# Performance work log

Measured on AMD Instinct MI355X. Metric: run time of the kernel, lower is better.

Reference implementation:

```python
import jax, jax.numpy as jnp
import numpy as np


def _cdist(x, y):
    # Euclidean pairwise distances, (N,D) x (M,D) -> (N,M)
    x2 = jnp.sum(x * x, axis=1, keepdims=True)          # (N,1)
    y2 = jnp.sum(y * y, axis=1, keepdims=True).T        # (1,M)
    sq = x2 + y2 - 2.0 * (x @ y.T)
    return jnp.sqrt(jnp.maximum(sq, 0.0))


def setup_inputs() -> dict:
    key = jax.random.key(0)
    k1, k2, k3, k4 = jax.random.split(key, 4)
    return {
        "pred_feat": jax.random.normal(k1, (8192, 6), dtype=jnp.float32),
        "pred_decoder": jax.random.normal(k2, (4096, 4), dtype=jnp.float32),
        "input_data": jax.random.normal(k3, (4096, 4), dtype=jnp.float32),
        "gt_data": jax.random.normal(k4, (32768, 6), dtype=jnp.float32),
    }


def _repulsion_loss(pred_points, alpha=100.0, margin=0.3):
    N = pred_points.shape[0]
    d = _cdist(pred_points, pred_points)                # (N,N)
    eye = jnp.eye(N, dtype=d.dtype)
    d_no_self = d + 1e6 * eye
    min_dist = jnp.min(d_no_self, axis=1)               # (N,)
    penalty = jax.nn.softplus(alpha * (margin - min_dist))
    return jnp.mean(penalty ** 2)


def reference(pred_feat, pred_decoder, input_data, gt_data):
    # train_decoder=False branch of CombinedCriterionAEImpulse.forward
    pred_points = pred_feat[:, :3]
    pred_normals = pred_feat[:, 3:]
    gt_points = gt_data[:, :3]
    gt_normals = gt_data[:, 3:]

    # nearest-neighbor matching: NxL cdist + argmin + gather
    dists = _cdist(pred_points, gt_points)              # (N,L)
    min_indices = jnp.argmin(dists, axis=1)             # (N,)
    closest_gt_points = gt_points[min_indices]          # (N,3)

    attraction_loss = jnp.mean((pred_points - closest_gt_points) ** 2)
    repulsion = _repulsion_loss(pred_points)
    inlier_loss = attraction_loss + repulsion

    # normal alignment loss
    closest_gt_normals = gt_normals[min_indices]        # (N,3)
    eps = 1e-05
    pn = pred_normals / jnp.maximum(
        jnp.linalg.norm(pred_normals, axis=1, keepdims=True), eps)
    gn = closest_gt_normals / jnp.maximum(
        jnp.linalg.norm(closest_gt_normals, axis=1, keepdims=True), eps)
    cos_theta = jnp.sum(pn * gn, axis=1)
    norm_loss = jnp.mean(1.0 - cos_theta)

    combined_loss = inlier_loss + norm_loss * 10.0
    return combined_loss
```

## Files before the change

kernel.cpp:

```cpp
#include <hip/hip_runtime.h>
#include <cstdint>

typedef unsigned short ushort_t;
typedef unsigned int u32;
typedef unsigned long long u64;
typedef __attribute__((ext_vector_type(8))) short bf16x8;
typedef __attribute__((ext_vector_type(16))) float f32x16;

#define N_PRED 8192
#define N_GT   32768

#define NN_WAVES  4096
#define ALL_WAVES 5120

#define O_PRA  1048576u
#define O_PRB  1310720u
#define O_KNN  1572864u
#define O_KRP  5767168u
#define O_PART 6815744u

__device__ __forceinline__ float max3f(float a, float b, float c) {
    float d;
    asm("v_max3_f32 %0, %1, %2, %3" : "=v"(d) : "v"(a), "v"(b), "v"(c));
    return d;
}
__device__ __forceinline__ ushort_t f2b(float v) {
    u32 b = __float_as_uint(v);
    return (ushort_t)((b + 0x7FFFu + ((b >> 16) & 1u)) >> 16);
}
__device__ __forceinline__ u32 packf(float v) {
    const u32 b = __float_as_uint(v);
    return b ^ ((u32)((int)b >> 31) | 0x80000000u);
}

#define LATCH(ACC, B, K, T)                                        \
    {                                                              \
        const float _m0 = max3f(ACC[0], ACC[1], ACC[2]);           \
        const float _m1 = max3f(ACC[3], ACC[4], ACC[5]);           \
        const float _m2 = max3f(ACC[6], ACC[7], ACC[8]);           \
        const float _m3 = max3f(ACC[9], ACC[10], ACC[11]);         \
        const float _m4 = max3f(ACC[12], ACC[13], ACC[14]);        \
        const float _m5 = max3f(_m0, _m1, ACC[15]);                \
        const float _m6 = max3f(_m2, _m3, _m4);                    \
        const float _gm = fmaxf(_m5, _m6);                         \
        K = (_gm > B) ? (u32)(T) : K;                              \
        B = fmaxf(B, _gm);                                         \
    }

#define MASKROW(ACC)                                               \
    {                                                              \
        _Pragma("unroll")                                          \
        for (int _r = 0; _r < 16; ++_r) {                          \
            const int _row = (_r & 3) + 8 * (_r >> 2) + rowoff;    \
            ACC[_r] = (_row == col) ? -3.0e38f : ACC[_r];          \
        }                                                          \
    }

__global__ __launch_bounds__(256) void k_prep(const float* __restrict__ pred,
                                              const float* __restrict__ gt,
                                              ushort_t* __restrict__ gtA,
                                              ushort_t* __restrict__ prA,
                                              ushort_t* __restrict__ prB) {
    const int i = blockIdx.x * 256 + threadIdx.x;
    if (i < N_GT) {
        const float x = gt[i * 6 + 0], y = gt[i * 6 + 1], z = gt[i * 6 + 2];
        const ushort_t xh = f2b(x), yh = f2b(y), zh = f2b(z);
        const ushort_t xl = f2b(x - __uint_as_float((u32)xh << 16));
        const ushort_t yl = f2b(y - __uint_as_float((u32)yh << 16));
        const ushort_t zl = f2b(z - __uint_as_float((u32)zh << 16));
        const float w = -0.5f * fmaf(z, z, fmaf(y, y, x * x));
        const ushort_t wh = f2b(w);
        const ushort_t wl = f2b(w - __uint_as_float((u32)wh << 16));
        ushort_t* d = gtA + (i >> 5) * 512 + (i & 31) * 8;
        d[0] = xh; d[1] = yh; d[2] = zh; d[3] = xh; d[4] = yh; d[5] = zh; d[6] = xl; d[7] = yl;
        d += 256;
        d[0] = zl; d[1] = wh; d[2] = wl; d[3] = 0; d[4] = 0; d[5] = 0; d[6] = 0; d[7] = 0;
    }
    if (i < N_PRED) {
        const float x = pred[i * 6 + 0], y = pred[i * 6 + 1], z = pred[i * 6 + 2];
        const ushort_t xh = f2b(x), yh = f2b(y), zh = f2b(z);
        const ushort_t xl = f2b(x - __uint_as_float((u32)xh << 16));
        const ushort_t yl = f2b(y - __uint_as_float((u32)yh << 16));
        const ushort_t zl = f2b(z - __uint_as_float((u32)zh << 16));
        const float w = -0.5f * fmaf(z, z, fmaf(y, y, x * x));
        const ushort_t wh = f2b(w);
        const ushort_t wl = f2b(w - __uint_as_float((u32)wh << 16));
        ushort_t* a = prA + (i >> 5) * 512 + (i & 31) * 8;
        a[0] = xh; a[1] = yh; a[2] = zh; a[3] = xh; a[4] = yh; a[5] = zh; a[6] = xl; a[7] = yl;
        a += 256;
        a[0] = zl; a[1] = wh; a[2] = wl; a[3] = 0; a[4] = 0; a[5] = 0; a[6] = 0; a[7] = 0;
        const ushort_t ONE = 0x3F80;
        ushort_t* b = prB + (i >> 5) * 512 + (i & 31) * 8;
        b[0] = xh; b[1] = yh; b[2] = zh; b[3] = xl; b[4] = yl; b[5] = zl; b[6] = xh; b[7] = yh;
        b += 256;
        b[0] = zh; b[1] = ONE; b[2] = ONE; b[3] = 0; b[4] = 0; b[5] = 0; b[6] = 0; b[7] = 0;
    }
}

template <bool DIAG>
__device__ __forceinline__ void scan16(const bf16x8* __restrict__ ap,
                                       const bf16x8 B0, const bf16x8 B1,
                                       const bf16x8 B2, const bf16x8 B3,
                                       const int ts0, const int ts1,
                                       const int ts2, const int ts3,
                                       const int col, const int rowoff,
                                       float& b0, float& b1, float& b2, float& b3,
                                       u32& k0, u32& k1, u32& k2, u32& k3) {
    const f32x16 zc = {};
    bf16x8 Aa = ap[0];
    bf16x8 Ab = ap[64];
#pragma unroll
    for (int t = 0; t < 16; ++t) {
        const int tn = (t + 2 < 16) ? t + 2 : 15;
        const bf16x8 An = ap[tn * 64];
        f32x16 accA = __builtin_amdgcn_mfma_f32_32x32x16_bf16(Aa, B0, zc, 0, 0, 0);
        f32x16 accB = __builtin_amdgcn_mfma_f32_32x32x16_bf16(Aa, B1, zc, 0, 0, 0);
        if (DIAG && t == ts0) MASKROW(accA);
        LATCH(accA, b0, k0, t);
        accA = __builtin_amdgcn_mfma_f32_32x32x16_bf16(Aa, B2, zc, 0, 0, 0);
        if (DIAG && t == ts1) MASKROW(accB);
        LATCH(accB, b1, k1, t);
        accB = __builtin_amdgcn_mfma_f32_32x32x16_bf16(Aa, B3, zc, 0, 0, 0);
        if (DIAG && t == ts2) MASKROW(accA);
        LATCH(accA, b2, k2, t);
        if (DIAG && t == ts3) MASKROW(accB);
        LATCH(accB, b3, k3, t);
        Aa = Ab;
        Ab = An;
    }
}

__global__ __launch_bounds__(256) void k_pair(const ushort_t* __restrict__ gtA,
                                              const ushort_t* __restrict__ prA,
                                              const ushort_t* __restrict__ prB,
                                              u64* __restrict__ keysNN,
                                              u64* __restrict__ keysRP) {
    const int wid = blockIdx.x * 4 + (threadIdx.x >> 6);
    const int lane = threadIdx.x & 63;

    const bool isNN = (wid < NN_WAVES);
    const int rw = isNN ? wid : (wid - NN_WAVES);
    const int pg = rw & 63;
    const int sp = rw >> 6;

    const int lu = (lane >> 5) * 32 + (lane & 31);
    const int col = lane & 31;
    const int rowoff = (lane >> 5) * 4;

    const bf16x8* bp = (const bf16x8*)prB;
    const bf16x8 B0 = bp[(pg * 4 + 0) * 64 + lu];
    const bf16x8 B1 = bp[(pg * 4 + 1) * 64 + lu];
    const bf16x8 B2 = bp[(pg * 4 + 2) * 64 + lu];
    const bf16x8 B3 = bp[(pg * 4 + 3) * 64 + lu];

    const bf16x8* ap = (const bf16x8*)(isNN ? gtA : prA) + sp * 1024 + lu;

    float b0 = -3.0e38f, b1 = -3.0e38f, b2 = -3.0e38f, b3 = -3.0e38f;
    u32 k0 = 0, k1 = 0, k2 = 0, k3 = 0;

    const bool diag = (!isNN) && (sp == (pg >> 2));
    if (diag) {
        const int tb = (pg & 3) * 4;
        scan16<true>(ap, B0, B1, B2, B3, tb, tb + 1, tb + 2, tb + 3,
                     col, rowoff, b0, b1, b2, b3, k0, k1, k2, k3);
    } else {
        scan16<false>(ap, B0, B1, B2, B3, -1, -1, -1, -1,
                      col, rowoff, b0, b1, b2, b3, k0, k1, k2, k3);
    }

#define FOLD(B, K)                                                  \
    {                                                               \
        const float _ob = __shfl_xor(B, 32);                        \
        const u32 _ok = __shfl_xor(K, 32);                          \
        const bool _tk = (_ob > B) || (_ob == B && _ok < K);        \
        B = _tk ? _ob : B;                                          \
        K = _tk ? _ok : K;                                          \
    }
    FOLD(b0, k0); FOLD(b1, k1); FOLD(b2, k2); FOLD(b3, k3);
#undef FOLD

    if (lane < 32) {
        u64* keys = isNN ? keysNN : keysRP;
        const int Pb = pg * 128 + col;
        const u32 tb = (u32)(sp * 16);
        keys[(size_t)sp * N_PRED + Pb +  0] = ((u64)packf(b0) << 32) | (u64)(~(tb + k0));
        keys[(size_t)sp * N_PRED + Pb + 32] = ((u64)packf(b1) << 32) | (u64)(~(tb + k1));
        keys[(size_t)sp * N_PRED + Pb + 64] = ((u64)packf(b2) << 32) | (u64)(~(tb + k2));
        keys[(size_t)sp * N_PRED + Pb + 96] = ((u64)packf(b3) << 32) | (u64)(~(tb + k3));
    }
}

__global__ __launch_bounds__(256) void k_fin(const float* __restrict__ pred,
                                             const float* __restrict__ gt,
                                             const u64* __restrict__ keysNN,
                                             const u64* __restrict__ keysRP,
                                             float* __restrict__ partials) {
    const int wave = threadIdx.x >> 6;
    const int lane = threadIdx.x & 63;
    const int p = blockIdx.x * 4 + wave;

    const float px = pred[p * 6 + 0], py = pred[p * 6 + 1], pz = pred[p * 6 + 2];

    u64 kv = keysNN[(size_t)lane * N_PRED + p];
#pragma unroll
    for (int off = 32; off > 0; off >>= 1) {
        const u64 o = __shfl_xor(kv, off);
        kv = (o > kv) ? o : kv;
    }
    const u32 tile = ~((u32)kv);
    {
    }
    const int g = (int)tile * 32 + (lane & 31);
    float bh;
    int bj;
    {
        const float x = gt[g * 6 + 0], y = gt[g * 6 + 1], z = gt[g * 6 + 2];
        const float w = -0.5f * fmaf(z, z, fmaf(y, y, x * x));
        bh = fmaf(px, x, fmaf(py, y, fmaf(pz, z, w)));
        bj = g;
    }
#pragma unroll
    for (int off = 32; off > 0; off >>= 1) {
        const float oh = __shfl_xor(bh, off);
        const int og = __shfl_xor(bj, off);
        const bool take = (oh > bh) || (oh == bh && og < bj);
        bh = take ? oh : bh;
        bj = take ? og : bj;
    }
    const int j = bj;

    u64 rv = (lane < 16) ? keysRP[(size_t)lane * N_PRED + p] : 0ull;
#pragma unroll
    for (int off = 32; off > 0; off >>= 1) {
        const u64 o = __shfl_xor(rv, off);
        rv = (o > rv) ? o : rv;
    }
    const u32 tile2 = ~((u32)rv);
    const int q = (int)tile2 * 32 + (lane & 31);
    float hr;
    {
        const float x = pred[q * 6 + 0], y = pred[q * 6 + 1], z = pred[q * 6 + 2];
        const float w = -0.5f * fmaf(z, z, fmaf(y, y, x * x));
        float h = fmaf(px, x, fmaf(py, y, fmaf(pz, z, w)));
        hr = (q == p) ? -3.0e38f : h;
    }
#pragma unroll
    for (int off = 32; off > 0; off >>= 1) hr = fmaxf(hr, __shfl_xor(hr, off));

    __shared__ float red[4][3];
    if (lane == 0) {
        const float gx = gt[j * 6 + 0], gy = gt[j * 6 + 1], gz = gt[j * 6 + 2];
        const float dx = px - gx, dy = py - gy, dz = pz - gz;
        const float att = dx * dx + dy * dy + dz * dz;

        const float pnx = pred[p * 6 + 3], pny = pred[p * 6 + 4], pnz = pred[p * 6 + 5];
        const float gnx = gt[j * 6 + 3],   gny = gt[j * 6 + 4],   gnz = gt[j * 6 + 5];
        const float pl = fmaxf(sqrtf(pnx * pnx + pny * pny + pnz * pnz), 1e-5f);
        const float gl = fmaxf(sqrtf(gnx * gnx + gny * gny + gnz * gnz), 1e-5f);
        const float nrm = 1.0f - (pnx * gnx + pny * gny + pnz * gnz) / (pl * gl);

        const float pp2 = px * px + py * py + pz * pz;
        float d2 = fmaf(-2.0f, hr, pp2);
        d2 = fmaxf(d2, 0.0f);
        const float xa = 100.0f * (0.3f - sqrtf(d2));
        const float sp2 = fmaxf(xa, 0.0f) + log1pf(expf(-fabsf(xa)));

        red[wave][0] = att;
        red[wave][1] = nrm;
        red[wave][2] = sp2 * sp2;
    }
    __syncthreads();
    if (threadIdx.x < 3)
        partials[blockIdx.x * 3 + threadIdx.x] =
            red[0][threadIdx.x] + red[1][threadIdx.x] +
            red[2][threadIdx.x] + red[3][threadIdx.x];
}

__device__ __forceinline__ float wave_reduce(float v) {
#pragma unroll
    for (int off = 32; off > 0; off >>= 1) v += __shfl_down(v, off, 64);
    return v;
}

__global__ __launch_bounds__(256) void k_comb(const float* __restrict__ partials,
                                              float* __restrict__ out) {
    float a = 0.f, n = 0.f, r = 0.f;
    const int t = threadIdx.x;
#pragma unroll
    for (int k = 0; k < 8; ++k) {
        const int row = t + k * 256;
        a += partials[row * 3 + 0];
        n += partials[row * 3 + 1];
        r += partials[row * 3 + 2];
    }
    a = wave_reduce(a);
    n = wave_reduce(n);
    r = wave_reduce(r);
    __shared__ float red[3][4];
    const int wave = t >> 6, lane = t & 63;
    if (lane == 0) { red[0][wave] = a; red[1][wave] = n; red[2][wave] = r; }
    __syncthreads();
    if (t == 0) {
        const float A = red[0][0] + red[0][1] + red[0][2] + red[0][3];
        const float Nn = red[1][0] + red[1][1] + red[1][2] + red[1][3];
        const float R = red[2][0] + red[2][1] + red[2][2] + red[2][3];
        out[0] = A / (float)(N_PRED * 3) + R / (float)N_PRED + 10.0f * (Nn / (float)N_PRED);
    }
}

extern "C" void kernel_launch(void* const* d_in, const int* in_sizes, int n_in,
                              void* d_out, int out_size, void* d_ws, size_t ws_size,
                              hipStream_t stream) {
    const float* pred = (const float*)d_in[0];
    const float* gt   = (const float*)d_in[3];
    float* out = (float*)d_out;
    char* ws = (char*)d_ws;

    ushort_t* gtA = (ushort_t*)ws;
    ushort_t* prA = (ushort_t*)(ws + O_PRA);
    ushort_t* prB = (ushort_t*)(ws + O_PRB);
    u64* keysNN = (u64*)(ws + O_KNN);
    u64* keysRP = (u64*)(ws + O_KRP);
    float* partials = (float*)(ws + O_PART);

    k_prep<<<N_GT / 256, 256, 0, stream>>>(pred, gt, gtA, prA, prB);
    k_pair<<<ALL_WAVES / 4, 256, 0, stream>>>(gtA, prA, prB, keysNN, keysRP);
    k_fin<<<N_PRED / 4, 256, 0, stream>>>(pred, gt, keysNN, keysRP, partials);
    k_comb<<<1, 256, 0, stream>>>(partials, out);
}
```

Measured before the change: 42.33 us.

## Track argmax per 4-tile group in MFMA scan and rescan 128 candidates

The MFMA scan no longer records the best tile after every 32-wide tile. It reduces four tiles into a running max using max3 and records only the group index, which removes the compare and select from the inner loop. The finishing kernel now recomputes exact distances over 128 candidates (two per lane) instead of 32, trading more gather work in k_fin for a leaner hot loop. The A-operand prefetch depth drops from two to one, which may expose load latency.

```diff
diff --git a/kernel.cpp b/kernel.cpp
--- a/kernel.cpp
+++ b/kernel.cpp
@@ -32,20 +32,16 @@
     const u32 b = __float_as_uint(v);
     return b ^ ((u32)((int)b >> 31) | 0x80000000u);
 }
-
-#define LATCH(ACC, B, K, T)                                        \
-    {                                                              \
-        const float _m0 = max3f(ACC[0], ACC[1], ACC[2]);           \
-        const float _m1 = max3f(ACC[3], ACC[4], ACC[5]);           \
-        const float _m2 = max3f(ACC[6], ACC[7], ACC[8]);           \
-        const float _m3 = max3f(ACC[9], ACC[10], ACC[11]);         \
-        const float _m4 = max3f(ACC[12], ACC[13], ACC[14]);        \
-        const float _m5 = max3f(_m0, _m1, ACC[15]);                \
-        const float _m6 = max3f(_m2, _m3, _m4);                    \
-        const float _gm = fmaxf(_m5, _m6);                         \
-        K = (_gm > B) ? (u32)(T) : K;                              \
-        B = fmaxf(B, _gm);                                         \
-    }
+__device__ __forceinline__ float red16(const f32x16 a, float best) {
+    const float m0 = max3f(a[0], a[1], a[2]);
+    const float m1 = max3f(a[3], a[4], a[5]);
+    const float m2 = max3f(a[6], a[7], a[8]);
+    const float m3 = max3f(a[9], a[10], a[11]);
+    const float m4 = max3f(a[12], a[13], a[14]);
+    const float m5 = max3f(m0, m1, a[15]);
+    const float m6 = max3f(m2, m3, m4);
+    return max3f(best, m5, m6);
+}
 
 #define MASKROW(ACC)                                               \
     {                                                              \
@@ -107,26 +103,32 @@
                                        float& b0, float& b1, float& b2, float& b3,
                                        u32& k0, u32& k1, u32& k2, u32& k3) {
     const f32x16 zc = {};
-    bf16x8 Aa = ap[0];
-    bf16x8 Ab = ap[64];
-#pragma unroll
-    for (int t = 0; t < 16; ++t) {
-        const int tn = (t + 2 < 16) ? t + 2 : 15;
-        const bf16x8 An = ap[tn * 64];
-        f32x16 accA = __builtin_amdgcn_mfma_f32_32x32x16_bf16(Aa, B0, zc, 0, 0, 0);
-        f32x16 accB = __builtin_amdgcn_mfma_f32_32x32x16_bf16(Aa, B1, zc, 0, 0, 0);
-        if (DIAG && t == ts0) MASKROW(accA);
-        LATCH(accA, b0, k0, t);
-        accA = __builtin_amdgcn_mfma_f32_32x32x16_bf16(Aa, B2, zc, 0, 0, 0);
-        if (DIAG && t == ts1) MASKROW(accB);
-        LATCH(accB, b1, k1, t);
-        accB = __builtin_amdgcn_mfma_f32_32x32x16_bf16(Aa, B3, zc, 0, 0, 0);
-        if (DIAG && t == ts2) MASKROW(accA);
-        LATCH(accA, b2, k2, t);
-        if (DIAG && t == ts3) MASKROW(accB);
-        LATCH(accB, b3, k3, t);
-        Aa = Ab;
-        Ab = An;
+    bf16x8 Acur = ap[0];
+#pragma unroll
+    for (int G = 0; G < 4; ++G) {
+        float g0 = -3.0e38f, g1 = -3.0e38f, g2 = -3.0e38f, g3 = -3.0e38f;
+#pragma unroll
+        for (int tt = 0; tt < 4; ++tt) {
+            const int t = G * 4 + tt;
+            const bf16x8 Anxt = (t < 15) ? ap[(t + 1) * 64] : Acur;
+            f32x16 accA = __builtin_amdgcn_mfma_f32_32x32x16_bf16(Acur, B0, zc, 0, 0, 0);
+            f32x16 accB = __builtin_amdgcn_mfma_f32_32x32x16_bf16(Acur, B1, zc, 0, 0, 0);
+            if (DIAG && t == ts0) MASKROW(accA);
+            g0 = red16(accA, g0);
+            accA = __builtin_amdgcn_mfma_f32_32x32x16_bf16(Acur, B2, zc, 0, 0, 0);
+            if (DIAG && t == ts1) MASKROW(accB);
+            g1 = red16(accB, g1);
+            accB = __builtin_amdgcn_mfma_f32_32x32x16_bf16(Acur, B3, zc, 0, 0, 0);
+            if (DIAG && t == ts2) MASKROW(accA);
+            g2 = red16(accA, g2);
+            if (DIAG && t == ts3) MASKROW(accB);
+            g3 = red16(accB, g3);
+            Acur = Anxt;
+        }
+        k0 = (g0 > b0) ? (u32)G : k0;  b0 = fmaxf(b0, g0);
+        k1 = (g1 > b1) ? (u32)G : k1;  b1 = fmaxf(b1, g1);
+        k2 = (g2 > b2) ? (u32)G : k2;  b2 = fmaxf(b2, g2);
+        k3 = (g3 > b3) ? (u32)G : k3;  b3 = fmaxf(b3, g3);
     }
 }
 
@@ -143,17 +145,16 @@
     const int pg = rw & 63;
     const int sp = rw >> 6;
 
-    const int lu = (lane >> 5) * 32 + (lane & 31);
     const int col = lane & 31;
     const int rowoff = (lane >> 5) * 4;
 
     const bf16x8* bp = (const bf16x8*)prB;
-    const bf16x8 B0 = bp[(pg * 4 + 0) * 64 + lu];
-    const bf16x8 B1 = bp[(pg * 4 + 1) * 64 + lu];
-    const bf16x8 B2 = bp[(pg * 4 + 2) * 64 + lu];
-    const bf16x8 B3 = bp[(pg * 4 + 3) * 64 + lu];
-
-    const bf16x8* ap = (const bf16x8*)(isNN ? gtA : prA) + sp * 1024 + lu;
+    const bf16x8 B0 = bp[(pg * 4 + 0) * 64 + lane];
+    const bf16x8 B1 = bp[(pg * 4 + 1) * 64 + lane];
+    const bf16x8 B2 = bp[(pg * 4 + 2) * 64 + lane];
+    const bf16x8 B3 = bp[(pg * 4 + 3) * 64 + lane];
+
+    const bf16x8* ap = (const bf16x8*)(isNN ? gtA : prA) + sp * 1024 + lane;
 
     float b0 = -3.0e38f, b1 = -3.0e38f, b2 = -3.0e38f, b3 = -3.0e38f;
     u32 k0 = 0, k1 = 0, k2 = 0, k3 = 0;
@@ -182,11 +183,11 @@
     if (lane < 32) {
         u64* keys = isNN ? keysNN : keysRP;
         const int Pb = pg * 128 + col;
-        const u32 tb = (u32)(sp * 16);
-        keys[(size_t)sp * N_PRED + Pb +  0] = ((u64)packf(b0) << 32) | (u64)(~(tb + k0));
-        keys[(size_t)sp * N_PRED + Pb + 32] = ((u64)packf(b1) << 32) | (u64)(~(tb + k1));
-        keys[(size_t)sp * N_PRED + Pb + 64] = ((u64)packf(b2) << 32) | (u64)(~(tb + k2));
-        keys[(size_t)sp * N_PRED + Pb + 96] = ((u64)packf(b3) << 32) | (u64)(~(tb + k3));
+        const u32 gb = (u32)(sp * 4);
+        keys[(size_t)sp * N_PRED + Pb +  0] = ((u64)packf(b0) << 32) | (u64)(~(gb + k0));
+        keys[(size_t)sp * N_PRED + Pb + 32] = ((u64)packf(b1) << 32) | (u64)(~(gb + k1));
+        keys[(size_t)sp * N_PRED + Pb + 64] = ((u64)packf(b2) << 32) | (u64)(~(gb + k2));
+        keys[(size_t)sp * N_PRED + Pb + 96] = ((u64)packf(b3) << 32) | (u64)(~(gb + k3));
     }
 }
 
@@ -207,17 +208,16 @@
         const u64 o = __shfl_xor(kv, off);
         kv = (o > kv) ? o : kv;
     }
-    const u32 tile = ~((u32)kv);
-    {
-    }
-    const int g = (int)tile * 32 + (lane & 31);
-    float bh;
-    int bj;
-    {
+    const int G = (int)(~(u32)kv);
+    float bh = -3.0e38f;
+    int bj = 0x7FFFFFFF;
+#pragma unroll
+    for (int i = 0; i < 2; ++i) {
+        const int g = G * 128 + i * 64 + lane;
         const float x = gt[g * 6 + 0], y = gt[g * 6 + 1], z = gt[g * 6 + 2];
         const float w = -0.5f * fmaf(z, z, fmaf(y, y, x * x));
-        bh = fmaf(px, x, fmaf(py, y, fmaf(pz, z, w)));
-        bj = g;
+        const float h = fmaf(px, x, fmaf(py, y, fmaf(pz, z, w)));
+        if (h > bh) { bh = h; bj = g; }
     }
 #pragma unroll
     for (int off = 32; off > 0; off >>= 1) {
@@ -235,14 +235,16 @@
         const u64 o = __shfl_xor(rv, off);
         rv = (o > rv) ? o : rv;
     }
-    const u32 tile2 = ~((u32)rv);
-    const int q = (int)tile2 * 32 + (lane & 31);
-    float hr;
-    {
+    const int G2 = (int)(~(u32)rv);
+    float hr = -3.0e38f;
+#pragma unroll
+    for (int i = 0; i < 2; ++i) {
+        const int q = G2 * 128 + i * 64 + lane;
         const float x = pred[q * 6 + 0], y = pred[q * 6 + 1], z = pred[q * 6 + 2];
         const float w = -0.5f * fmaf(z, z, fmaf(y, y, x * x));
         float h = fmaf(px, x, fmaf(py, y, fmaf(pz, z, w)));
-        hr = (q == p) ? -3.0e38f : h;
+        h = (q == p) ? -3.0e38f : h;
+        hr = fmaxf(hr, h);
     }
 #pragma unroll
     for (int off = 32; off > 0; off >>= 1) hr = fmaxf(hr, __shfl_xor(hr, off));
```

After: 39.59 us. -6.5%, faster.
